# Performance work log

Hardware: AMD Instinct MI355X
Metric: run time of the kernel (lower is better)

Reference implementation:

```python
import jax, jax.numpy as jnp
import numpy as np

B, D_IN, H, C = 8192, 2048, 1024, 1000
LAYERS = [0, 1, 2, 3, 4]          # structure.layers
N_MAIN = 4                        # main hidden layers for layers[1:]
# skip layers in __init__ enumeration order: (target_layer, source_layer)
SKIPS = [(2, 0), (3, 0), (3, 1), (4, 0), (4, 1), (4, 2)]


def _linear_init(key, out_f, in_f):
    k1, k2 = jax.random.split(key)
    bound = 1.0 / np.sqrt(in_f)
    W = jax.random.uniform(k1, (out_f, in_f), minval=-bound, maxval=bound, dtype=jnp.float32)
    b = jax.random.uniform(k2, (out_f,), minval=-bound, maxval=bound, dtype=jnp.float32)
    return W, b


def setup_inputs() -> dict:
    key = jax.random.key(0)
    ks = iter(jax.random.split(key, 40))
    x = jax.random.normal(next(ks), (B, D_IN), dtype=jnp.float32)

    Wf, bf = _linear_init(next(ks), H, D_IN)
    mf = jax.random.bernoulli(next(ks), 0.5, (H, D_IN))

    main_W, main_b, main_m = [], [], []
    for _ in range(N_MAIN):
        W, b = _linear_init(next(ks), H, H)
        main_W.append(W); main_b.append(b)
        main_m.append(jax.random.bernoulli(next(ks), 0.5, (H, H)))

    skip_W, skip_b, skip_m = [], [], []
    for _ in SKIPS:
        W, b = _linear_init(next(ks), H, H)
        skip_W.append(W); skip_b.append(b)
        skip_m.append(jax.random.bernoulli(next(ks), 0.5, (H, H)))

    Wo, bo = _linear_init(next(ks), C, H)
    mo = jax.random.bernoulli(next(ks), 0.5, (C, H))

    return {"x": x, "Wf": Wf, "bf": bf, "mf": mf,
            "main_W": main_W, "main_b": main_b, "main_m": main_m,
            "skip_W": skip_W, "skip_b": skip_b, "skip_m": skip_m,
            "Wo": Wo, "bo": bo, "mo": mo}


def _masked_linear(x, W, b, m):
    # F.linear(x, weight * mask, bias): mask applied to weight before GEMM
    return x @ (W * m).T + b


def reference(x, Wf, bf, mf, main_W, main_b, main_m, skip_W, skip_b, skip_m, Wo, bo, mo):
    relu = jax.nn.relu
    last = relu(_masked_linear(x, Wf, bf, mf))        # layer 0 output, [B, H]
    results = {0: last}
    for i, layer_idx in enumerate(LAYERS[1:]):
        out = relu(_masked_linear(last, main_W[i], main_b[i], main_m[i]))
        for k, (tgt, src) in enumerate(SKIPS):
            if tgt == layer_idx:
                out = out + relu(_masked_linear(results[src], skip_W[k], skip_b[k], skip_m[k]))
        results[layer_idx] = out
        last = out
    return _masked_linear(last, Wo, bo, mo)            # [B, C]
```

## Files before the change

kernel.cpp:

```cpp
#include <hip/hip_runtime.h>
#include <hip/hip_bf16.h>
#include <stdint.h>


typedef unsigned short ushort_t;
typedef __bf16 bf16x8 __attribute__((ext_vector_type(8)));
typedef float f32x4 __attribute__((ext_vector_type(4)));

__device__ __forceinline__ void gl_lds16(const void* g, void* l) {
  typedef __attribute__((address_space(1))) void gvoid;
  typedef __attribute__((address_space(3))) void lvoid;
  __builtin_amdgcn_global_load_lds((gvoid*)(void*)g, (lvoid*)l, 16, 0, 0);
}

__device__ __forceinline__ ushort_t f2b(float f) {
  __hip_bfloat16 h = (__hip_bfloat16)f;
  return *(ushort_t*)&h;
}

__global__ void detect_kernel(const ushort_t* x, const ushort_t* mf, int* flags) {
  __shared__ int s[4];
  if (threadIdx.x < 4) s[threadIdx.x] = 0;
  __syncthreads();
  int expout = 0, m3f80_even = 0, m3f80_odd = 0, mhi01 = 0;
  for (int k = threadIdx.x; k < 2048; k += 256) {
    ushort_t w = x[k];
    int e = (w >> 7) & 0xFF;
    if (e < 96 || e > 144) expout++;
    ushort_t mw = mf[k];
    if (mw == 0x3F80) { if (k & 1) m3f80_odd++; else m3f80_even++; }
    if ((mw >> 8) == 1) mhi01++;
  }
  atomicAdd(&s[0], expout);
  atomicAdd(&s[1], m3f80_even);
  atomicAdd(&s[2], m3f80_odd);
  atomicAdd(&s[3], mhi01);
  __syncthreads();
  if (threadIdx.x == 0) {
    flags[0] = (s[0] > 100) ? 1 : 0;
    int mmode = 0;
    if (s[1] > 100) mmode = 2;
    else if (s[2] > 100) mmode = 3;
    else if (s[3] > 200) mmode = 1;
    flags[1] = mmode;
  }
}

struct PrepEnt {
  const void* w; size_t woff;
  const void* m; size_t moff;
  ushort_t* o;
  int n;
  int valid;
};
struct PrepAll { PrepEnt e[25]; };

__global__ void prep_weights(PrepAll p, const int* flags) {
  const bool f32 = flags[0] != 0;
  const int mmode = flags[1];
  const PrepEnt e = p.e[blockIdx.y];
  const int nch = e.n >> 3;
  const int stride = blockDim.x * gridDim.x;
  for (int ci = blockIdx.x * blockDim.x + threadIdx.x; ci < nch; ci += stride) {
    const int i = ci << 3;
    ushort_t o[8] = {0, 0, 0, 0, 0, 0, 0, 0};
    if (i < e.valid) {
      ushort_t wb[8];
      if (f32) {
        const float* wp = (const float*)e.w + e.woff + i;
        float4 a = *(const float4*)wp;
        float4 b = *(const float4*)(wp + 4);
        wb[0] = f2b(a.x); wb[1] = f2b(a.y); wb[2] = f2b(a.z); wb[3] = f2b(a.w);
        wb[4] = f2b(b.x); wb[5] = f2b(b.y); wb[6] = f2b(b.z); wb[7] = f2b(b.w);
      } else {
        *(uint4*)wb = *(const uint4*)((const ushort_t*)e.w + e.woff + i);
      }
      unsigned mk = 0xFF;
      if (e.m) {
        mk = 0;
        if (mmode == 0) {
          const int4* mp = (const int4*)((const int*)e.m + e.moff + i);
          int4 a = mp[0], b = mp[1];
          mk = (a.x != 0) | ((a.y != 0) << 1) | ((a.z != 0) << 2) | ((a.w != 0) << 3) |
               ((b.x != 0) << 4) | ((b.y != 0) << 5) | ((b.z != 0) << 6) | ((b.w != 0) << 7);
        } else if (mmode == 1) {
          const uint2 mv = *(const uint2*)((const unsigned char*)e.m + e.moff + i);
          const unsigned char* mb = (const unsigned char*)&mv;
          for (int j = 0; j < 8; j++) mk |= (mb[j] != 0) << j;
        } else if (mmode == 2) {
          uint4 mv = *(const uint4*)((const ushort_t*)e.m + e.moff + i);
          const ushort_t* ms = (const ushort_t*)&mv;
          for (int j = 0; j < 8; j++) mk |= (ms[j] != 0) << j;
        } else {
          const uint4* mp = (const uint4*)((const unsigned int*)e.m + e.moff + i);
          uint4 a = mp[0], b = mp[1];
          const unsigned* u = (const unsigned*)&a;
          const unsigned* v = (const unsigned*)&b;
          for (int j = 0; j < 4; j++) mk |= (u[j] != 0) << j;
          for (int j = 0; j < 4; j++) mk |= (v[j] != 0) << (4 + j);
        }
      }
#pragma unroll
      for (int j = 0; j < 8; j++) o[j] = ((mk >> j) & 1) ? wb[j] : (ushort_t)0;
    }
    *(uint4*)(e.o + i) = *(uint4*)o;
  }
}

struct GemmSrc { const ushort_t* A; const ushort_t* B; const ushort_t* bias; };
struct GemmArgs { GemmSrc s[4]; };

#define SBAR()  asm volatile("s_barrier" ::: "memory")
#define LGKM0() asm volatile("s_waitcnt lgkmcnt(0)" ::: "memory")
#define VMC6()  asm volatile("s_waitcnt vmcnt(6)" ::: "memory")
#define VMC0()  asm volatile("s_waitcnt vmcnt(0)" ::: "memory")

template <int NSRC, bool RELU, bool NGUARD>
__launch_bounds__(512, 2)
__global__ void gemm_multi(GemmArgs args, void* Cv, const int* of32flag,
                           int K, int N_real, int ldc)
{
  __shared__ __align__(16) ushort_t lds[2][24576];

  const bool of32 = (of32flag != nullptr) && (of32flag[0] != 0);
  __hip_bfloat16* C = (__hip_bfloat16*)Cv;
  float* Cf = (float*)Cv;

  const int tid  = threadIdx.x;
  const int lane = tid & 63;
  const int wave = tid >> 6;
  const int wm = (wave >> 1) * 64;
  const int wn = (wave & 1) * 64;
  const int fr = lane & 15;
  const int kg = lane >> 4;

  const int lid = blockIdx.x;
  const int xcd = lid & 7, chunk = lid >> 3;
  const int bm = (xcd * 4 + (chunk >> 3)) * 256;
  const int bn = (chunk & 7) * 128;

  const int rbase = tid >> 3;
  const int sg    = (tid & 7) ^ (rbase & 7);
  const size_t aoff = (size_t)(bm + rbase) * K + sg * 8;
  const size_t boff = (size_t)(bn + rbase) * K + sg * 8;
  const size_t rs64 = (size_t)64 * K;

  auto stage = [&](const ushort_t* gA, const ushort_t* gB, int buf) {
    ushort_t* base = &lds[buf][0];
    ushort_t* lA = base + wave * 512;
    ushort_t* lB = base + 16384 + wave * 512;
    gl_lds16(gA,            lA);
    gl_lds16(gA + rs64,     lA + 4096);
    gl_lds16(gA + 2 * rs64, lA + 8192);
    gl_lds16(gA + 3 * rs64, lA + 12288);
    gl_lds16(gB,            lB);
    gl_lds16(gB + rs64,     lB + 4096);
  };

  const int s0   = (kg ^ (fr & 7)) * 16;
  const int arow = (wm + fr) * 128;
  const int brow = 32768 + (wn + fr) * 128;

  f32x4 acc[4][4], out_acc[4][4];
#pragma unroll
  for (int i = 0; i < 4; i++)
#pragma unroll
    for (int j = 0; j < 4; j++) {
      acc[i][j] = (f32x4){0.f, 0.f, 0.f, 0.f};
      if (NSRC > 1) out_acc[i][j] = (f32x4){0.f, 0.f, 0.f, 0.f};
    }

  float bpre[NSRC][4];
#pragma unroll
  for (int s = 0; s < NSRC; ++s)
#pragma unroll
    for (int ni = 0; ni < 4; ni++)
      bpre[s][ni] = (float)*(const __hip_bfloat16*)
          (args.s[s].bias + bn + wn + ni * 16 + fr);

  const int TPS = K >> 6;
  const int NT  = TPS * NSRC;

  stage(args.s[0].A + aoff, args.s[0].B + boff, 0);
  {
    const int s1 = 1 / TPS, k1 = (1 % TPS) * 64;
    stage(args.s[s1].A + aoff + k1, args.s[s1].B + boff + k1, 1);
  }
  VMC6();
  SBAR();

  int psrc = 2 / TPS, pk0 = (2 % TPS) * 64;
  int csrc = 0, ck = 0;
  int cur = 0;

  for (int t = 0; t < NT; ++t) {
    const char* Lb = (const char*)&lds[cur][0];

    bf16x8 af[4][2], bfr[4][2];
#pragma unroll
    for (int m = 0; m < 4; ++m)
#pragma unroll
      for (int ks = 0; ks < 2; ++ks)
        af[m][ks] = *(const bf16x8*)(Lb + arow + m * 2048 + (s0 ^ (ks * 64)));
#pragma unroll
    for (int n = 0; n < 4; ++n)
#pragma unroll
      for (int ks = 0; ks < 2; ++ks)
        bfr[n][ks] = *(const bf16x8*)(Lb + brow + n * 2048 + (s0 ^ (ks * 64)));

    __builtin_amdgcn_s_setprio(1);
#pragma unroll
    for (int mi = 0; mi < 4; mi++)
#pragma unroll
      for (int ni = 0; ni < 4; ni++)
#pragma unroll
        for (int ks = 0; ks < 2; ++ks)
          acc[mi][ni] = __builtin_amdgcn_mfma_f32_16x16x32_bf16(
              af[mi][ks], bfr[ni][ks], acc[mi][ni], 0, 0, 0);
    __builtin_amdgcn_s_setprio(0);

    LGKM0();
    SBAR();

    ck += 64;
    const bool srcEnd = (ck == K);
    const bool more2 = (t + 2 < NT);
    if (more2) {
      stage(args.s[psrc].A + aoff + pk0, args.s[psrc].B + boff + pk0, cur);
      pk0 += 64; if (pk0 == K) { pk0 = 0; ++psrc; }
    }

    if (NSRC > 1 && srcEnd) {
      float bb[4];
#pragma unroll
      for (int s = 0; s < NSRC; ++s)
        if (s == csrc) {
#pragma unroll
          for (int ni = 0; ni < 4; ni++) bb[ni] = bpre[s][ni];
        }
#pragma unroll
      for (int ni = 0; ni < 4; ni++)
#pragma unroll
        for (int mi = 0; mi < 4; mi++)
#pragma unroll
          for (int j = 0; j < 4; j++) {
            float v = acc[mi][ni][j] + bb[ni];
            if (RELU) v = fmaxf(v, 0.0f);
            out_acc[mi][ni][j] += v;
            acc[mi][ni][j] = 0.0f;
          }
      ck = 0; ++csrc;
    }

    if (t + 1 < NT) {
      if (more2) VMC6(); else VMC0();
      SBAR();
    }
    cur ^= 1;
  }

#pragma unroll
  for (int ni = 0; ni < 4; ni++) {
    const int c = bn + wn + ni * 16 + fr;
    if (NGUARD && c >= N_real) continue;
#pragma unroll
    for (int mi = 0; mi < 4; mi++) {
      const int r0 = bm + wm + mi * 16 + kg * 4;
#pragma unroll
      for (int j = 0; j < 4; j++) {
        const size_t idx = (size_t)(r0 + j) * ldc + c;
        float v;
        if (NSRC == 1) {
          v = acc[mi][ni][j] + bpre[0][ni];
          if (RELU) v = fmaxf(v, 0.0f);
        } else {
          v = out_acc[mi][ni][j];
        }
        if (of32) Cf[idx] = v;
        else      C[idx]  = (__hip_bfloat16)v;
      }
    }
  }
}

extern "C" void kernel_launch(void* const* d_in, const int* in_sizes, int n_in,
                              void* d_out, int out_size, void* d_ws, size_t ws_size,
                              hipStream_t stream) {
  (void)out_size; (void)ws_size;
  const int Bm = 8192, DIN = 2048, H = 1024, Cn = 1000;
  const size_t HH = (size_t)H * H;

  struct PO { const void* p; size_t off; };
  PO x{d_in[0], 0}, Wf{d_in[0], 0}, mf{d_in[0], 0}, Wo{d_in[0], 0}, mo{d_in[0], 0};
  PO bf{d_in[0], 0}, bo{d_in[0], 0};
  PO mW[4], mM[4], mB[4], sW[6], sM[6], sB[6];
  for (int i = 0; i < 4; i++) { mW[i] = {d_in[0], 0}; mM[i] = mW[i]; mB[i] = mW[i]; }
  for (int i = 0; i < 6; i++) { sW[i] = {d_in[0], 0}; sM[i] = sW[i]; sB[i] = sW[i]; }

  {
    int c2M = 0, c1M = 0, c1k = 0, cWoMo = 0, c4 = 0, c6 = 0;
    for (int i = 0; i < n_in; i++) {
      const int s = in_sizes[i];
      const void* p = d_in[i];
      switch (s) {
        case 16777216: x = {p, 0}; break;
        case 2097152:  if (c2M++ == 0) Wf = {p, 0}; else mf = {p, 0}; break;
        case 1048576: {
          int j = c1M++;
          if (j < 4)       mW[j]      = {p, 0};
          else if (j < 8)  mM[j - 4]  = {p, 0};
          else if (j < 14) sW[j - 8]  = {p, 0};
          else if (j < 20) sM[j - 14] = {p, 0};
          break;
        }
        case 1024: {
          int j = c1k++;
          if (j == 0)      bf        = {p, 0};
          else if (j < 5)  mB[j - 1] = {p, 0};
          else if (j < 11) sB[j - 5] = {p, 0};
          break;
        }
        case 1024000: if (cWoMo++ == 0) Wo = {p, 0}; else mo = {p, 0}; break;
        case 1000: bo = {p, 0}; break;
        case 4194304:
          for (int t = 0; t < 4; t++) {
            if (c4 == 0) mW[t] = {p, t * HH}; else mM[t] = {p, t * HH};
          }
          c4++; break;
        case 6291456:
          for (int t = 0; t < 6; t++) {
            if (c6 == 0) sW[t] = {p, t * HH}; else sM[t] = {p, t * HH};
          }
          c6++; break;
        case 4096:
          for (int t = 0; t < 4; t++) mB[t] = {p, (size_t)t * H};
          break;
        case 6144:
          for (int t = 0; t < 6; t++) sB[t] = {p, (size_t)t * H};
          break;
        default: break;
      }
    }
  }

  ushort_t* wsp = (ushort_t*)d_ws;
  size_t off = 0;
  int* flags = (int*)wsp; off += 32;
  ushort_t* xc = wsp + off; off += (size_t)Bm * DIN;
  __hip_bfloat16* r[5];
  for (int i = 0; i < 5; i++) { r[i] = (__hip_bfloat16*)(wsp + off); off += (size_t)Bm * H; }
  ushort_t* wWf = wsp + off; off += (size_t)H * DIN;
  ushort_t* wMain[4];
  for (int i = 0; i < 4; i++) { wMain[i] = wsp + off; off += HH; }
  ushort_t* wSkip[6];
  for (int k = 0; k < 6; k++) { wSkip[k] = wsp + off; off += HH; }
  ushort_t* wWo = wsp + off; off += (size_t)1024 * 1024;
  ushort_t* cbf_ = wsp + off; off += 1024;
  ushort_t* cmB[4];
  for (int i = 0; i < 4; i++) { cmB[i] = wsp + off; off += 1024; }
  ushort_t* csB[6];
  for (int k = 0; k < 6; k++) { csB[k] = wsp + off; off += 1024; }
  ushort_t* cbo = wsp + off; off += 1024;

  detect_kernel<<<1, 256, 0, stream>>>((const ushort_t*)x.p, (const ushort_t*)mf.p, flags);

  PrepAll p;
  p.e[0]  = { Wf.p, Wf.off, mf.p, mf.off, wWf, H * DIN, H * DIN };
  for (int i = 0; i < 4; i++)
    p.e[1 + i] = { mW[i].p, mW[i].off, mM[i].p, mM[i].off, wMain[i], (int)HH, (int)HH };
  for (int k = 0; k < 6; k++)
    p.e[5 + k] = { sW[k].p, sW[k].off, sM[k].p, sM[k].off, wSkip[k], (int)HH, (int)HH };
  p.e[11] = { Wo.p, Wo.off, mo.p, mo.off, wWo, 1024 * 1024, Cn * H };
  p.e[12] = { bf.p, bf.off, nullptr, 0, cbf_, H, H };
  for (int i = 0; i < 4; i++)
    p.e[13 + i] = { mB[i].p, mB[i].off, nullptr, 0, cmB[i], H, H };
  for (int k = 0; k < 6; k++)
    p.e[17 + k] = { sB[k].p, sB[k].off, nullptr, 0, csB[k], H, H };
  p.e[23] = { bo.p, bo.off, nullptr, 0, cbo, 1024, Cn };
  p.e[24] = { x.p, x.off, nullptr, 0, xc, Bm * DIN, Bm * DIN };
  prep_weights<<<dim3(256, 25), dim3(256), 0, stream>>>(p, flags);

  const dim3 g(256), b(512);

  GemmArgs a0; a0.s[0] = { xc, wWf, cbf_ };
  gemm_multi<1, true, false><<<g, b, 0, stream>>>(a0, r[0], nullptr, DIN, H, H);

  GemmArgs a1; a1.s[0] = { (ushort_t*)r[0], wMain[0], cmB[0] };
  gemm_multi<1, true, false><<<g, b, 0, stream>>>(a1, r[1], nullptr, H, H, H);

  GemmArgs a2;
  a2.s[0] = { (ushort_t*)r[1], wMain[1], cmB[1] };
  a2.s[1] = { (ushort_t*)r[0], wSkip[0], csB[0] };
  gemm_multi<2, true, false><<<g, b, 0, stream>>>(a2, r[2], nullptr, H, H, H);

  GemmArgs a3;
  a3.s[0] = { (ushort_t*)r[2], wMain[2], cmB[2] };
  a3.s[1] = { (ushort_t*)r[0], wSkip[1], csB[1] };
  a3.s[2] = { (ushort_t*)r[1], wSkip[2], csB[2] };
  gemm_multi<3, true, false><<<g, b, 0, stream>>>(a3, r[3], nullptr, H, H, H);

  GemmArgs a4;
  a4.s[0] = { (ushort_t*)r[3], wMain[3], cmB[3] };
  a4.s[1] = { (ushort_t*)r[0], wSkip[3], csB[3] };
  a4.s[2] = { (ushort_t*)r[1], wSkip[4], csB[4] };
  a4.s[3] = { (ushort_t*)r[2], wSkip[5], csB[5] };
  gemm_multi<4, true, false><<<g, b, 0, stream>>>(a4, r[4], nullptr, H, H, H);

  GemmArgs ao; ao.s[0] = { (ushort_t*)r[4], wWo, cbo };
  gemm_multi<1, false, true><<<g, b, 0, stream>>>(ao, d_out, flags, H, Cn, Cn);
}
```

Baseline: 535.4 us.

## Software-pipeline LDS fragment reads against MFMA across k-halves and tiles

```diff
diff --git a/kernel.cpp b/kernel.cpp
--- a/kernel.cpp
+++ b/kernel.cpp
@@ -181,6 +181,43 @@
   const int TPS = K >> 6;
   const int NT  = TPS * NSRC;
 
+  bf16x8 af0[4], bf0[4], af1[4], bf1[4];
+
+  auto rdfrag0 = [&](const char* Lb, int ks) {
+    const int so = s0 ^ (ks * 64);
+#pragma unroll
+    for (int m = 0; m < 4; ++m) af0[m] = *(const bf16x8*)(Lb + arow + m * 2048 + so);
+#pragma unroll
+    for (int n = 0; n < 4; ++n) bf0[n] = *(const bf16x8*)(Lb + brow + n * 2048 + so);
+  };
+  auto rdfrag1 = [&](const char* Lb, int ks) {
+    const int so = s0 ^ (ks * 64);
+#pragma unroll
+    for (int m = 0; m < 4; ++m) af1[m] = *(const bf16x8*)(Lb + arow + m * 2048 + so);
+#pragma unroll
+    for (int n = 0; n < 4; ++n) bf1[n] = *(const bf16x8*)(Lb + brow + n * 2048 + so);
+  };
+  auto mfma16_0 = [&]() {
+    __builtin_amdgcn_s_setprio(1);
+#pragma unroll
+    for (int mi = 0; mi < 4; mi++)
+#pragma unroll
+      for (int ni = 0; ni < 4; ni++)
+        acc[mi][ni] = __builtin_amdgcn_mfma_f32_16x16x32_bf16(
+            af0[mi], bf0[ni], acc[mi][ni], 0, 0, 0);
+    __builtin_amdgcn_s_setprio(0);
+  };
+  auto mfma16_1 = [&]() {
+    __builtin_amdgcn_s_setprio(1);
+#pragma unroll
+    for (int mi = 0; mi < 4; mi++)
+#pragma unroll
+      for (int ni = 0; ni < 4; ni++)
+        acc[mi][ni] = __builtin_amdgcn_mfma_f32_16x16x32_bf16(
+            af1[mi], bf1[ni], acc[mi][ni], 0, 0, 0);
+    __builtin_amdgcn_s_setprio(0);
+  };
+
   stage(args.s[0].A + aoff, args.s[0].B + boff, 0);
   {
     const int s1 = 1 / TPS, k1 = (1 % TPS) * 64;
@@ -188,6 +225,7 @@
   }
   VMC6();
   SBAR();
+  rdfrag0((const char*)&lds[0][0], 0);
 
   int psrc = 2 / TPS, pk0 = (2 % TPS) * 64;
   int csrc = 0, ck = 0;
@@ -196,28 +234,9 @@
   for (int t = 0; t < NT; ++t) {
     const char* Lb = (const char*)&lds[cur][0];
 
-    bf16x8 af[4][2], bfr[4][2];
-#pragma unroll
-    for (int m = 0; m < 4; ++m)
-#pragma unroll
-      for (int ks = 0; ks < 2; ++ks)
-        af[m][ks] = *(const bf16x8*)(Lb + arow + m * 2048 + (s0 ^ (ks * 64)));
-#pragma unroll
-    for (int n = 0; n < 4; ++n)
-#pragma unroll
-      for (int ks = 0; ks < 2; ++ks)
-        bfr[n][ks] = *(const bf16x8*)(Lb + brow + n * 2048 + (s0 ^ (ks * 64)));
-
-    __builtin_amdgcn_s_setprio(1);
-#pragma unroll
-    for (int mi = 0; mi < 4; mi++)
-#pragma unroll
-      for (int ni = 0; ni < 4; ni++)
-#pragma unroll
-        for (int ks = 0; ks < 2; ++ks)
-          acc[mi][ni] = __builtin_amdgcn_mfma_f32_16x16x32_bf16(
-              af[mi][ks], bfr[ni][ks], acc[mi][ni], 0, 0, 0);
-    __builtin_amdgcn_s_setprio(0);
+    rdfrag1(Lb, 1);
+    __builtin_amdgcn_sched_barrier(0);
+    mfma16_0();
 
     LGKM0();
     SBAR();
@@ -229,6 +248,14 @@
       stage(args.s[psrc].A + aoff + pk0, args.s[psrc].B + boff + pk0, cur);
       pk0 += 64; if (pk0 == K) { pk0 = 0; ++psrc; }
     }
+
+    if (t + 1 < NT) {
+      if (more2) VMC6(); else VMC0();
+      SBAR();
+      rdfrag0((const char*)&lds[cur ^ 1][0], 0);
+    }
+    __builtin_amdgcn_sched_barrier(0);
+    mfma16_1();
 
     if (NSRC > 1 && srcEnd) {
       float bb[4];
@@ -252,10 +279,6 @@
       ck = 0; ++csrc;
     }
 
-    if (t + 1 < NT) {
-      if (more2) VMC6(); else VMC0();
-      SBAR();
-    }
     cur ^= 1;
   }
 
```

New measurement: 529.8 us. No clear change (-1.0%).
